# Performance work log

Measured on AMD Instinct MI355X. Metric: run time of the kernel, lower is better.

## Reference

```python
import jax, jax.numpy as jnp
import numpy as np

N = 10000        # nodes
E = 160000       # edges (before self loops)
F_IN = 4         # n_features
D = 128          # d_model (per-head out channels for GAT, GCN width)
H = 8            # n_heads
NEG_SLOPE = 0.2  # PyG GATConv default leaky relu slope


def setup_inputs() -> dict:
    key = jax.random.key(0)
    ks = jax.random.split(key, 10)
    x = jax.random.normal(ks[0], (N, F_IN), dtype=jnp.float32)
    edge_index = jax.random.randint(ks[1], (2, E), 0, N, dtype=jnp.int64)
    s = 0.05
    gat_w = jax.random.normal(ks[2], (F_IN, H * D), dtype=jnp.float32) * s
    att_src = jax.random.normal(ks[3], (H, D), dtype=jnp.float32) * s
    att_dst = jax.random.normal(ks[4], (H, D), dtype=jnp.float32) * s
    gat_b = jnp.zeros((H * D,), dtype=jnp.float32)
    gcn1_w = jax.random.normal(ks[5], (H * D, D), dtype=jnp.float32) * s
    gcn1_b = jnp.zeros((D,), dtype=jnp.float32)
    gcn2_w = jax.random.normal(ks[6], (D, D), dtype=jnp.float32) * s
    gcn2_b = jnp.zeros((D,), dtype=jnp.float32)
    return {"x": x, "edge_index": edge_index, "gat_w": gat_w,
            "att_src": att_src, "att_dst": att_dst, "gat_b": gat_b,
            "gcn1_w": gcn1_w, "gcn1_b": gcn1_b,
            "gcn2_w": gcn2_w, "gcn2_b": gcn2_b}


def _add_self_loops(edge_index, n):
    loops = jnp.arange(n, dtype=edge_index.dtype)
    src = jnp.concatenate([edge_index[0], loops])
    dst = jnp.concatenate([edge_index[1], loops])
    return src, dst


def _gat_conv(x, src, dst, w, att_src, att_dst, b):
    # PyG GATConv, concat=True: h [N,H,D]
    h = (x @ w).reshape(-1, H, D)
    a_s = jnp.einsum('nhd,hd->nh', h, att_src)   # per-node src score
    a_d = jnp.einsum('nhd,hd->nh', h, att_dst)   # per-node dst score
    e = jax.nn.leaky_relu(a_s[src] + a_d[dst], NEG_SLOPE)  # [Etot,H]
    # segment softmax over destination node, per head
    m = jax.ops.segment_max(e, dst, num_segments=N)
    ex = jnp.exp(e - m[dst])
    denom = jax.ops.segment_sum(ex, dst, num_segments=N)
    alpha = ex / denom[dst]                       # [Etot,H]
    msg = h[src] * alpha[:, :, None]              # [Etot,H,D]
    out = jax.ops.segment_sum(msg, dst, num_segments=N)  # [N,H,D]
    return out.reshape(-1, H * D) + b


def _gcn_conv(x, src, dst, w, b):
    # PyG GCNConv with symmetric normalization (self loops already added)
    h = x @ w
    deg = jax.ops.segment_sum(jnp.ones_like(dst, dtype=h.dtype), dst,
                              num_segments=N)
    dinv = jnp.where(deg > 0, jax.lax.rsqrt(deg), 0.0)
    norm = dinv[src] * dinv[dst]                  # [Etot]
    out = jax.ops.segment_sum(h[src] * norm[:, None], dst, num_segments=N)
    return out + b


def reference(x, edge_index, gat_w, att_src, att_dst, gat_b,
              gcn1_w, gcn1_b, gcn2_w, gcn2_b):
    src, dst = _add_self_loops(edge_index, N)
    h = _gat_conv(x, src, dst, gat_w, att_src, att_dst, gat_b)
    h = jax.nn.gelu(h, approximate=False)         # torch F.gelu is exact erf
    h = _gcn_conv(h, src, dst, gcn1_w, gcn1_b)
    h = jax.nn.gelu(h, approximate=False)
    h = _gcn_conv(h, src, dst, gcn2_w, gcn2_b)
    return h                                      # [N, D]
```

## Files before the change

### kernel.cpp

```cpp
#include <hip/hip_runtime.h>
#include <math.h>

#define HEADS 8
#define DHEAD 128
#define CMODEL 1024
#define BCAP 64

typedef __attribute__((ext_vector_type(8))) short bf16x8;
typedef __attribute__((ext_vector_type(4))) float f32x4;

__device__ __forceinline__ float gelu_exact(float x) {
    return 0.5f * x * (1.0f + erff(x * 0.70710678118654752440f));
}

__device__ __forceinline__ unsigned short f2bf(float f) {
    unsigned u = __float_as_uint(f);
    return (unsigned short)((u + 0x7FFFu + ((u >> 16) & 1u)) >> 16);
}
__device__ __forceinline__ float bf2f(unsigned short h) {
    return __uint_as_float((unsigned)h << 16);
}

__global__ void __launch_bounds__(256) k_scores(const float* __restrict__ x,
                                                const float* __restrict__ gat_w,
                                                const float* __restrict__ att_src,
                                                const float* __restrict__ att_dst,
                                                const float* __restrict__ W1,
                                                const float* __restrict__ W2,
                                                float* __restrict__ xpack,
                                                float* __restrict__ a_d,
                                                int* __restrict__ cursor,
                                                unsigned short* __restrict__ W1hi,
                                                unsigned short* __restrict__ W1lo,
                                                unsigned short* __restrict__ W2hi,
                                                unsigned short* __restrict__ W2lo,
                                                int n_nodes, int nb_scores) {
    if ((int)blockIdx.x >= nb_scores) {
        int t = (blockIdx.x - nb_scores) * 256 + threadIdx.x;
        const int total1 = (1024 >> 5) * 8 * 64;
        const int total2 = (128 >> 5) * 8 * 64;
        const float* W; unsigned short *Whi, *Wlo;
        if (t < total1) { W = W1; Whi = W1hi; Wlo = W1lo; }
        else if (t < total1 + total2) { t -= total1; W = W2; Whi = W2hi; Wlo = W2lo; }
        else return;
        int lane = t & 63;
        int ct = (t >> 6) & 7;
        int kc = t >> 9;
        int quad = lane >> 4;
        int col = ct * 16 + (lane & 15);
        size_t o = (size_t)t * 8;
        #pragma unroll
        for (int j = 0; j < 8; j++) {
            float w = W[(size_t)(kc * 32 + quad * 8 + j) * 128 + col];
            unsigned short h = f2bf(w);
            Whi[o + j] = h;
            Wlo[o + j] = f2bf(w - bf2f(h));
        }
        return;
    }
    __shared__ float ws_s[32], ws_d[32];
    int t = threadIdx.x;
    if (t < 64) {
        int e = t >> 1;
        int which = t & 1;
        int hh = e >> 2, k = e & 3;
        const float* wrow = gat_w + k * CMODEL + hh * DHEAD;
        const float* av = which ? (att_dst + hh * DHEAD) : (att_src + hh * DHEAD);
        float s = 0.0f;
        for (int c = 0; c < DHEAD; c++) s += wrow[c] * av[c];
        if (which) ws_d[e] = s; else ws_s[e] = s;
    }
    int gid = blockIdx.x * 256 + t;
    if (gid < n_nodes) cursor[gid] = 0;
    __syncthreads();
    int p = gid;
    if (p >= n_nodes * HEADS) return;
    int n = p >> 3, hh = p & 7;
    float4 xv = *(const float4*)(x + (size_t)n * 4);
    float4 ws = *(const float4*)&ws_s[hh * 4];
    float4 wd = *(const float4*)&ws_d[hh * 4];
    a_d[p] = xv.x * wd.x + xv.y * wd.y + xv.z * wd.z + xv.w * wd.w;
    xpack[(size_t)n * 16 + 4 + hh] =
        xv.x * ws.x + xv.y * ws.y + xv.z * ws.z + xv.w * ws.w;
    if (hh == 0) *(float4*)(xpack + (size_t)n * 16) = xv;
}

__global__ void __launch_bounds__(256) k_scatter(const int* __restrict__ ei,
                                                 int* __restrict__ cursor,
                                                 int* __restrict__ bucket,
                                                 int n_nodes, int n_edges) {
    int e = blockIdx.x * 256 + threadIdx.x;
    int etot = n_edges + n_nodes;
    if (e >= etot) return;
    int s, d;
    if (e < n_edges) { s = ei[e]; d = ei[n_edges + e]; }
    else             { s = d = e - n_edges; }
    int pos = atomicAdd(&cursor[d], 1);
    if (pos < BCAP) bucket[(d << 6) + pos] = s;
}

__global__ void __launch_bounds__(256) k_smax_mm1(const float* __restrict__ xpack,
                                                  const float* __restrict__ a_d,
                                                  const int* __restrict__ deg,
                                                  const int* __restrict__ bucket,
                                                  const float* __restrict__ gat_w,
                                                  const float* __restrict__ gat_b,
                                                  const unsigned short* __restrict__ Bhi,
                                                  const unsigned short* __restrict__ Blo,
                                                  float* __restrict__ t,
                                                  int n_nodes) {
    __shared__ float xs[16 * 32];
    __shared__ float ck[2][16 * 36];
    int mb = blockIdx.x;
    int tid = threadIdx.x;
    {
        int q = tid >> 1;
        int half = tid & 1;
        int ln = q >> 3, hh = q & 7;
        int n = mb * 16 + ln;
        float sum = 0.0f;
        float4 acc = make_float4(0, 0, 0, 0);
        if (n < n_nodes) {
            int dg = deg[n]; if (dg > BCAP) dg = BCAP;
            int base = n << 6;
            float ad = a_d[n * 8 + hh];
            int r = half;
            for (; r + 6 < dg; r += 8) {
                int s0 = bucket[base + r + 0], s1 = bucket[base + r + 2];
                int s2 = bucket[base + r + 4], s3 = bucket[base + r + 6];
                const float* p0 = xpack + (size_t)s0 * 16;
                const float* p1 = xpack + (size_t)s1 * 16;
                const float* p2 = xpack + (size_t)s2 * 16;
                const float* p3 = xpack + (size_t)s3 * 16;
                float e0 = p0[4 + hh] + ad, e1 = p1[4 + hh] + ad;
                float e2 = p2[4 + hh] + ad, e3 = p3[4 + hh] + ad;
                float4 x0 = *(const float4*)p0;
                float4 x1 = *(const float4*)p1;
                float4 x2 = *(const float4*)p2;
                float4 x3 = *(const float4*)p3;
                e0 = (e0 > 0.0f) ? e0 : 0.2f * e0;  float w0 = __expf(e0);
                e1 = (e1 > 0.0f) ? e1 : 0.2f * e1;  float w1 = __expf(e1);
                e2 = (e2 > 0.0f) ? e2 : 0.2f * e2;  float w2 = __expf(e2);
                e3 = (e3 > 0.0f) ? e3 : 0.2f * e3;  float w3 = __expf(e3);
                sum += w0 + w1 + w2 + w3;
                acc.x += w0 * x0.x + w1 * x1.x + w2 * x2.x + w3 * x3.x;
                acc.y += w0 * x0.y + w1 * x1.y + w2 * x2.y + w3 * x3.y;
                acc.z += w0 * x0.z + w1 * x1.z + w2 * x2.z + w3 * x3.z;
                acc.w += w0 * x0.w + w1 * x1.w + w2 * x2.w + w3 * x3.w;
            }
            for (; r < dg; r += 2) {
                int s = bucket[base + r];
                const float* ps = xpack + (size_t)s * 16;
                float e = ps[4 + hh] + ad;
                e = (e > 0.0f) ? e : 0.2f * e;
                float ex = __expf(e);
                float4 xv = *(const float4*)ps;
                sum += ex;
                acc.x += ex * xv.x; acc.y += ex * xv.y;
                acc.z += ex * xv.z; acc.w += ex * xv.w;
            }
        }
        sum   += __shfl_down(sum, 1);
        acc.x += __shfl_down(acc.x, 1);
        acc.y += __shfl_down(acc.y, 1);
        acc.z += __shfl_down(acc.z, 1);
        acc.w += __shfl_down(acc.w, 1);
        if (half == 0) {
            float inv = (sum > 0.0f) ? (1.0f / sum) : 0.0f;
            *(float4*)&xs[q * 4] = make_float4(acc.x * inv, acc.y * inv,
                                               acc.z * inv, acc.w * inv);
        }
    }
    __syncthreads();
    int lane = tid & 63;
    int w = tid >> 6;
    int lm = lane & 15, quad = lane >> 4;
    int cc = tid & 31;
    int rp = tid >> 5;
    f32x4 macc[2];
    macc[0] = (f32x4){0.0f, 0.0f, 0.0f, 0.0f};
    macc[1] = (f32x4){0.0f, 0.0f, 0.0f, 0.0f};
    for (int kc = 0; kc < 32; kc++) {
        int buf = kc & 1;
        int col = kc * 32 + cc;
        int hh2 = col >> 7;
        float w0 = gat_w[col], w1 = gat_w[1024 + col],
              w2 = gat_w[2048 + col], w3 = gat_w[3072 + col];
        float bb = gat_b[col];
        #pragma unroll
        for (int rr = 0; rr < 2; rr++) {
            int row = rp * 2 + rr;
            float4 xa = *(const float4*)&xs[(row * 8 + hh2) * 4];
            float v = xa.x * w0 + xa.y * w1 + xa.z * w2 + xa.w * w3 + bb;
            ck[buf][row * 36 + cc] = gelu_exact(v);
        }
        __syncthreads();
        float a[8];
        *(float4*)&a[0] = *(const float4*)&ck[buf][lm * 36 + quad * 8];
        *(float4*)&a[4] = *(const float4*)&ck[buf][lm * 36 + quad * 8 + 4];
        bf16x8 ah, al;
        #pragma unroll
        for (int j = 0; j < 8; j++) {
            unsigned short h = f2bf(a[j]);
            ah[j] = (short)h;
            al[j] = (short)f2bf(a[j] - bf2f(h));
        }
        #pragma unroll
        for (int ct = 0; ct < 2; ct++) {
            const unsigned short* bh_p = Bhi + (((size_t)(kc * 8 + w * 2 + ct)) * 64 + lane) * 8;
            const unsigned short* bl_p = Blo + (((size_t)(kc * 8 + w * 2 + ct)) * 64 + lane) * 8;
            bf16x8 bh = *(const bf16x8*)bh_p;
            bf16x8 bl = *(const bf16x8*)bl_p;
            macc[ct] = __builtin_amdgcn_mfma_f32_16x16x32_bf16(ah, bh, macc[ct], 0, 0, 0);
            macc[ct] = __builtin_amdgcn_mfma_f32_16x16x32_bf16(al, bh, macc[ct], 0, 0, 0);
            macc[ct] = __builtin_amdgcn_mfma_f32_16x16x32_bf16(ah, bl, macc[ct], 0, 0, 0);
        }
    }
    #pragma unroll
    for (int ct = 0; ct < 2; ct++) {
        int col = (w * 2 + ct) * 16 + lm;
        #pragma unroll
        for (int reg = 0; reg < 4; reg++) {
            int row = mb * 16 + quad * 4 + reg;
            if (row < n_nodes) {
                float dv = 1.0f / sqrtf((float)deg[row]);
                t[(size_t)row * 128 + col] = macc[ct][reg] * dv;
            }
        }
    }
}

__global__ void __launch_bounds__(256) k_mm_mfma(const unsigned short* __restrict__ Afrag_hi,
                                                 const unsigned short* __restrict__ Afrag_lo,
                                                 const unsigned short* __restrict__ Bhi,
                                                 const unsigned short* __restrict__ Blo,
                                                 const int* __restrict__ deg_scale,
                                                 float* __restrict__ outp,
                                                 int n_nodes, int n_mtiles, int kcn) {
    int lane = threadIdx.x & 63;
    int w = threadIdx.x >> 6;
    int colhalf = w >> 1;
    int mtile = blockIdx.x * 2 + (w & 1);
    if (mtile >= n_mtiles) return;

    int lm = lane & 15, quad = lane >> 4;
    f32x4 acc[4];
    #pragma unroll
    for (int ct = 0; ct < 4; ct++) acc[ct] = (f32x4){0.0f, 0.0f, 0.0f, 0.0f};

    const unsigned short* ah_p = Afrag_hi + ((size_t)mtile * kcn * 64 + lane) * 8;
    const unsigned short* al_p = Afrag_lo + ((size_t)mtile * kcn * 64 + lane) * 8;
    const unsigned short* bh_p = Bhi + ((size_t)(colhalf * 4) * 64 + lane) * 8;
    const unsigned short* bl_p = Blo + ((size_t)(colhalf * 4) * 64 + lane) * 8;

    #pragma unroll 4
    for (int kci = 0; kci < kcn; kci++) {
        bf16x8 ah = *(const bf16x8*)(ah_p + (size_t)kci * 512);
        bf16x8 al = *(const bf16x8*)(al_p + (size_t)kci * 512);
        #pragma unroll
        for (int ct = 0; ct < 4; ct++) {
            bf16x8 bh = *(const bf16x8*)(bh_p + (size_t)kci * 4096 + ct * 512);
            bf16x8 bl = *(const bf16x8*)(bl_p + (size_t)kci * 4096 + ct * 512);
            acc[ct] = __builtin_amdgcn_mfma_f32_16x16x32_bf16(ah, bh, acc[ct], 0, 0, 0);
            acc[ct] = __builtin_amdgcn_mfma_f32_16x16x32_bf16(al, bh, acc[ct], 0, 0, 0);
            acc[ct] = __builtin_amdgcn_mfma_f32_16x16x32_bf16(ah, bl, acc[ct], 0, 0, 0);
        }
    }
    #pragma unroll
    for (int ct = 0; ct < 4; ct++) {
        int col = (colhalf * 4 + ct) * 16 + lm;
        #pragma unroll
        for (int reg = 0; reg < 4; reg++) {
            int row = mtile * 16 + quad * 4 + reg;
            if (row < n_nodes) {
                float v = acc[ct][reg] * (1.0f / sqrtf((float)deg_scale[row]));
                outp[(size_t)row * 128 + col] = v;
            }
        }
    }
}

__global__ void __launch_bounds__(256) k_gcn_agg(const float* __restrict__ t,
                                                 const int* __restrict__ deg,
                                                 const int* __restrict__ bucket,
                                                 const float* __restrict__ bias,
                                                 float* __restrict__ outF,
                                                 unsigned short* __restrict__ outHi,
                                                 unsigned short* __restrict__ outLo,
                                                 int n_nodes, int mode) {
    int c = threadIdx.x & 31;
    int ln = threadIdx.x >> 5;
    int n = blockIdx.x * 8 + ln;
    int col0 = blockIdx.y * 64;
    if (n >= n_nodes) return;
    float2 acc = make_float2(0.0f, 0.0f);
    int dgt = deg[n];
    int dg = dgt > BCAP ? BCAP : dgt;
    int base = n << 6;
    int sa = bucket[base + c];
    int sb = bucket[base + 32 + c];
    const float* tp = t + col0 + c * 2;
    int d1 = dg > 32 ? 32 : dg;
    int r = 0;
    for (; r + 4 <= d1; r += 4) {
        int s0 = __shfl(sa, r + 0, 32);
        int s1 = __shfl(sa, r + 1, 32);
        int s2 = __shfl(sa, r + 2, 32);
        int s3 = __shfl(sa, r + 3, 32);
        float2 v0 = *(const float2*)(tp + (size_t)s0 * 128);
        float2 v1 = *(const float2*)(tp + (size_t)s1 * 128);
        float2 v2 = *(const float2*)(tp + (size_t)s2 * 128);
        float2 v3 = *(const float2*)(tp + (size_t)s3 * 128);
        acc.x += v0.x + v1.x + v2.x + v3.x;
        acc.y += v0.y + v1.y + v2.y + v3.y;
    }
    for (; r < d1; r++) {
        int s = __shfl(sa, r, 32);
        float2 v = *(const float2*)(tp + (size_t)s * 128);
        acc.x += v.x; acc.y += v.y;
    }
    for (; r < dg; r++) {
        int s = __shfl(sb, r - 32, 32);
        float2 v = *(const float2*)(tp + (size_t)s * 128);
        acc.x += v.x; acc.y += v.y;
    }
    float dn = 1.0f / sqrtf((float)dgt);
    int k = col0 + c * 2;
    float2 bb = *(const float2*)(bias + k);
    float vx = acc.x * dn + bb.x;
    float vy = acc.y * dn + bb.y;
    if (mode) {
        vx = gelu_exact(vx); vy = gelu_exact(vy);
        size_t o = (((size_t)(n >> 4) * 4 + (k >> 5)) * 64
                    + ((k >> 3) & 3) * 16 + (n & 15)) * 8 + (k & 7);
        unsigned short hx = f2bf(vx), hy = f2bf(vy);
        outHi[o] = hx; outHi[o + 1] = hy;
        outLo[o] = f2bf(vx - bf2f(hx));
        outLo[o + 1] = f2bf(vy - bf2f(hy));
    } else {
        *(float2*)(outF + (size_t)n * 128 + k) = make_float2(vx, vy);
    }
}

extern "C" void kernel_launch(void* const* d_in, const int* in_sizes, int n_in,
                              void* d_out, int out_size, void* d_ws, size_t ws_size,
                              hipStream_t stream) {
    const float* x        = (const float*)d_in[0];
    const int*   ei       = (const int*)d_in[1];
    const float* gat_w    = (const float*)d_in[2];
    const float* att_src  = (const float*)d_in[3];
    const float* att_dst  = (const float*)d_in[4];
    const float* gat_b    = (const float*)d_in[5];
    const float* gcn1_w   = (const float*)d_in[6];
    const float* gcn1_b   = (const float*)d_in[7];
    const float* gcn2_w   = (const float*)d_in[8];
    const float* gcn2_b   = (const float*)d_in[9];
    float* out = (float*)d_out;

    int N = in_sizes[0] / 4;
    int E = in_sizes[1] / 2;
    int Etot = E + N;
    int n_mtiles = (N + 15) / 16;

    char* base = (char*)d_ws;
    float*          t      = (float*)(base);
    float*          t2     = (float*)(base + 5120000);
    unsigned short* out2hi = (unsigned short*)(base + 10240000);
    unsigned short* out2lo = (unsigned short*)(base + 12800000);
    unsigned short* w1hi   = (unsigned short*)(base + 26000000);
    unsigned short* w1lo   = (unsigned short*)(base + 26262144);
    unsigned short* w2hi   = (unsigned short*)(base + 26524288);
    unsigned short* w2lo   = (unsigned short*)(base + 26557056);
    size_t off = 81920000;
    float* xpack  = (float*)(base + off); off += (size_t)N * 16 * 4;
    float* a_d    = (float*)(base + off); off += (size_t)N * 8 * 4;
    int*   cursor = (int*)(base + off);   off += (size_t)N * 4;
    int*   bucket = (int*)(base + off);   off += (size_t)N * BCAP * 4;

    int nb_scores = (N * HEADS + 255) / 256;
    int nb_wswz   = (16384 + 2048 + 255) / 256;

    k_scores<<<nb_scores + nb_wswz, 256, 0, stream>>>(x, gat_w, att_src, att_dst,
                                                      gcn1_w, gcn2_w, xpack, a_d, cursor,
                                                      w1hi, w1lo, w2hi, w2lo, N, nb_scores);

    k_scatter<<<(Etot + 255) / 256, 256, 0, stream>>>(ei, cursor, bucket, N, E);

    k_smax_mm1<<<n_mtiles, 256, 0, stream>>>(xpack, a_d, cursor, bucket,
                                             gat_w, gat_b, w1hi, w1lo, t, N);

    int nmb2 = (n_mtiles + 1) / 2;
    int nagg = (N + 7) / 8;

    k_gcn_agg<<<dim3(nagg, 2), 256, 0, stream>>>(t, cursor, bucket, gcn1_b,
                                                 nullptr, out2hi, out2lo, N, 1);

    k_mm_mfma<<<dim3(nmb2, 1), 256, 0, stream>>>(out2hi, out2lo, w2hi, w2lo,
                                                 cursor, t2, N, n_mtiles, 4);

    k_gcn_agg<<<dim3(nagg, 2), 256, 0, stream>>>(t2, cursor, bucket, gcn2_b,
                                                 out, nullptr, nullptr, N, 0);
}
```

Measured before the change: 163.6 us.

## Prefetch bucket and B fragments, widen GELU chunk to 64 columns

```diff
diff --git a/kernel.cpp b/kernel.cpp
--- a/kernel.cpp
+++ b/kernel.cpp
@@ -99,7 +99,7 @@
     if (pos < BCAP) bucket[(d << 6) + pos] = s;
 }
 
-__global__ void __launch_bounds__(256) k_smax_mm1(const float* __restrict__ xpack,
+__global__ void __launch_bounds__(256, 3) k_smax_mm1(const float* __restrict__ xpack,
                                                   const float* __restrict__ a_d,
                                                   const int* __restrict__ deg,
                                                   const int* __restrict__ bucket,
@@ -110,24 +110,48 @@
                                                   float* __restrict__ t,
                                                   int n_nodes) {
     __shared__ float xs[16 * 32];
-    __shared__ float ck[2][16 * 36];
+    __shared__ float ck[2][16 * 68];
     int mb = blockIdx.x;
     int tid = threadIdx.x;
+    int lane = tid & 63;
+    int w = tid >> 6;
+
+    bf16x8 bhA[2][2], blA[2][2], bhB[2][2], blB[2][2];
+    #pragma unroll
+    for (int kc2 = 0; kc2 < 2; kc2++)
+        #pragma unroll
+        for (int ct = 0; ct < 2; ct++) {
+            size_t bi = (((size_t)(kc2 * 8) + w * 2 + ct) * 64 + lane) * 8;
+            bhA[kc2][ct] = *(const bf16x8*)(Bhi + bi);
+            blA[kc2][ct] = *(const bf16x8*)(Blo + bi);
+        }
+
     {
         int q = tid >> 1;
         int half = tid & 1;
-        int ln = q >> 3, hh = q & 7;
+        int ln = tid >> 4, hh = q & 7;
         int n = mb * 16 + ln;
+        int nc = (n < n_nodes) ? n : (n_nodes - 1);
+        int grp = lane & 48;
+        int gl = lane & 15;
+        int basec = nc << 6;
+        int pre0 = bucket[basec + gl];
+        int pre1 = bucket[basec + 16 + gl];
+        int pre2 = bucket[basec + 32 + gl];
+        int pre3 = bucket[basec + 48 + gl];
+        auto SRC = [&](int e) -> int {
+            int v = (e < 16) ? pre0 : (e < 32) ? pre1 : (e < 48) ? pre2 : pre3;
+            return __shfl(v, grp + (e & 15), 64);
+        };
         float sum = 0.0f;
         float4 acc = make_float4(0, 0, 0, 0);
         if (n < n_nodes) {
             int dg = deg[n]; if (dg > BCAP) dg = BCAP;
-            int base = n << 6;
             float ad = a_d[n * 8 + hh];
             int r = half;
             for (; r + 6 < dg; r += 8) {
-                int s0 = bucket[base + r + 0], s1 = bucket[base + r + 2];
-                int s2 = bucket[base + r + 4], s3 = bucket[base + r + 6];
+                int s0 = SRC(r + 0), s1 = SRC(r + 2);
+                int s2 = SRC(r + 4), s3 = SRC(r + 6);
                 const float* p0 = xpack + (size_t)s0 * 16;
                 const float* p1 = xpack + (size_t)s1 * 16;
                 const float* p2 = xpack + (size_t)s2 * 16;
@@ -149,7 +173,7 @@
                 acc.w += w0 * x0.w + w1 * x1.w + w2 * x2.w + w3 * x3.w;
             }
             for (; r < dg; r += 2) {
-                int s = bucket[base + r];
+                int s = SRC(r);
                 const float* ps = xpack + (size_t)s * 16;
                 float e = ps[4 + hh] + ad;
                 e = (e > 0.0f) ? e : 0.2f * e;
@@ -172,50 +196,67 @@
         }
     }
     __syncthreads();
-    int lane = tid & 63;
-    int w = tid >> 6;
+
     int lm = lane & 15, quad = lane >> 4;
-    int cc = tid & 31;
-    int rp = tid >> 5;
+    int cc = tid & 63;
+    int rp = tid >> 6;
     f32x4 macc[2];
     macc[0] = (f32x4){0.0f, 0.0f, 0.0f, 0.0f};
     macc[1] = (f32x4){0.0f, 0.0f, 0.0f, 0.0f};
-    for (int kc = 0; kc < 32; kc++) {
-        int buf = kc & 1;
-        int col = kc * 32 + cc;
-        int hh2 = col >> 7;
-        float w0 = gat_w[col], w1 = gat_w[1024 + col],
-              w2 = gat_w[2048 + col], w3 = gat_w[3072 + col];
-        float bb = gat_b[col];
-        #pragma unroll
-        for (int rr = 0; rr < 2; rr++) {
-            int row = rp * 2 + rr;
-            float4 xa = *(const float4*)&xs[(row * 8 + hh2) * 4];
-            float v = xa.x * w0 + xa.y * w1 + xa.z * w2 + xa.w * w3 + bb;
-            ck[buf][row * 36 + cc] = gelu_exact(v);
-        }
-        __syncthreads();
-        float a[8];
-        *(float4*)&a[0] = *(const float4*)&ck[buf][lm * 36 + quad * 8];
-        *(float4*)&a[4] = *(const float4*)&ck[buf][lm * 36 + quad * 8 + 4];
-        bf16x8 ah, al;
-        #pragma unroll
-        for (int j = 0; j < 8; j++) {
-            unsigned short h = f2bf(a[j]);
-            ah[j] = (short)h;
-            al[j] = (short)f2bf(a[j] - bf2f(h));
-        }
-        #pragma unroll
-        for (int ct = 0; ct < 2; ct++) {
-            const unsigned short* bh_p = Bhi + (((size_t)(kc * 8 + w * 2 + ct)) * 64 + lane) * 8;
-            const unsigned short* bl_p = Blo + (((size_t)(kc * 8 + w * 2 + ct)) * 64 + lane) * 8;
-            bf16x8 bh = *(const bf16x8*)bh_p;
-            bf16x8 bl = *(const bf16x8*)bl_p;
-            macc[ct] = __builtin_amdgcn_mfma_f32_16x16x32_bf16(ah, bh, macc[ct], 0, 0, 0);
-            macc[ct] = __builtin_amdgcn_mfma_f32_16x16x32_bf16(al, bh, macc[ct], 0, 0, 0);
-            macc[ct] = __builtin_amdgcn_mfma_f32_16x16x32_bf16(ah, bl, macc[ct], 0, 0, 0);
-        }
-    }
+
+#define ROUND(RR, BH, BL, BH_N, BL_N, RNEXT)                                    \
+    {                                                                           \
+        int buf = (RR) & 1;                                                     \
+        int col = (RR) * 64 + cc;                                               \
+        float w0 = gat_w[col], w1 = gat_w[1024 + col],                          \
+              w2 = gat_w[2048 + col], w3 = gat_w[3072 + col];                   \
+        float bb = gat_b[col];                                                  \
+        int hh2 = (RR) >> 1;                                                    \
+        _Pragma("unroll")                                                       \
+        for (int rr = 0; rr < 4; rr++) {                                        \
+            int row = rp * 4 + rr;                                              \
+            float4 xa = *(const float4*)&xs[(row * 8 + hh2) * 4];               \
+            float v = xa.x * w0 + xa.y * w1 + xa.z * w2 + xa.w * w3 + bb;       \
+            ck[buf][row * 68 + cc] = gelu_exact(v);                             \
+        }                                                                       \
+        _Pragma("unroll")                                                       \
+        for (int kc2 = 0; kc2 < 2; kc2++)                                       \
+            _Pragma("unroll")                                                   \
+            for (int ct = 0; ct < 2; ct++) {                                    \
+                size_t bi = (((size_t)((RNEXT) * 2 + kc2) * 8 + w * 2 + ct) * 64 + lane) * 8; \
+                BH_N[kc2][ct] = *(const bf16x8*)(Bhi + bi);                     \
+                BL_N[kc2][ct] = *(const bf16x8*)(Blo + bi);                     \
+            }                                                                   \
+        asm volatile("s_waitcnt lgkmcnt(0)" ::: "memory");                      \
+        __builtin_amdgcn_s_barrier();                                           \
+        __builtin_amdgcn_sched_barrier(0);                                      \
+        _Pragma("unroll")                                                       \
+        for (int kc2 = 0; kc2 < 2; kc2++) {                                     \
+            float a[8];                                                         \
+            *(float4*)&a[0] = *(const float4*)&ck[buf][lm * 68 + kc2 * 32 + quad * 8];     \
+            *(float4*)&a[4] = *(const float4*)&ck[buf][lm * 68 + kc2 * 32 + quad * 8 + 4]; \
+            bf16x8 ah, al;                                                      \
+            _Pragma("unroll")                                                   \
+            for (int j = 0; j < 8; j++) {                                       \
+                unsigned short h = f2bf(a[j]);                                  \
+                ah[j] = (short)h;                                               \
+                al[j] = (short)f2bf(a[j] - bf2f(h));                            \
+            }                                                                   \
+            _Pragma("unroll")                                                   \
+            for (int ct = 0; ct < 2; ct++) {                                    \
+                macc[ct] = __builtin_amdgcn_mfma_f32_16x16x32_bf16(ah, BH[kc2][ct], macc[ct], 0, 0, 0); \
+                macc[ct] = __builtin_amdgcn_mfma_f32_16x16x32_bf16(al, BH[kc2][ct], macc[ct], 0, 0, 0); \
+                macc[ct] = __builtin_amdgcn_mfma_f32_16x16x32_bf16(ah, BL[kc2][ct], macc[ct], 0, 0, 0); \
+            }                                                                   \
+        }                                                                       \
+    }
+
+    for (int r = 0; r < 16; r += 2) {
+        ROUND(r,     bhA, blA, bhB, blB, r + 1);
+        ROUND(r + 1, bhB, blB, bhA, blA, (r + 2 < 16 ? r + 2 : 15));
+    }
+#undef ROUND
+
     #pragma unroll
     for (int ct = 0; ct < 2; ct++) {
         int col = (w * 2 + ct) * 16 + lm;
```

After: 157.0 us. 1.04x faster.
